# Kernel tuning notes

Measured on AMD Instinct MI355X. Metric: run time of the kernel, lower is better.

The kernel has to match this reference:

```python
import jax, jax.numpy as jnp
import numpy as np

NUM_HEADS = 16

def _rope(t, cos, sin):
    # t: [B,H,T,hd]; cos/sin: [T,half]
    half = t.shape[-1] // 2
    t1, t2 = t[..., :half], t[..., half:]
    return jnp.concatenate((t1 * cos - t2 * sin, t1 * sin + t2 * cos), axis=-1)

def setup_inputs() -> dict:
    key = jax.random.key(0)
    ks = jax.random.split(key, 5)
    B, T, D = 2, 2048, 2048
    s = 0.02
    return {
        'x': jax.random.normal(ks[0], (B, T, D), jnp.float32),
        'w_qkv': jax.random.normal(ks[1], (3 * D, D), jnp.float32) * s,
        'b_qkv': jax.random.normal(ks[2], (3 * D,), jnp.float32) * s,
        'w_out': jax.random.normal(ks[3], (D, D), jnp.float32) * s,
        'b_out': jax.random.normal(ks[4], (D,), jnp.float32) * s,
    }

def reference(x, w_qkv, b_qkv, w_out, b_out):
    B, T, D = x.shape
    H = NUM_HEADS
    hd = D // H
    half = hd // 2
    # fused QKV projection (torch Linear: x @ W^T + b)
    qkv = (x @ w_qkv.T + b_qkv).reshape(B, T, H, 3, hd)
    q, k, v = qkv[..., 0, :], qkv[..., 1, :], qkv[..., 2, :]
    q, k, v = (jnp.transpose(t, (0, 2, 1, 3)) for t in (q, k, v))  # [B,H,T,hd]
    # RoPE frequencies (buffer computed as in __init__)
    theta = 1.0 / (10000.0 ** (jnp.arange(half, dtype=jnp.float32) / half))
    freq = jnp.arange(T, dtype=jnp.float32)[:, None] * theta[None, :]  # [T,half]
    cos, sin = jnp.cos(freq), jnp.sin(freq)
    q = _rope(q, cos, sin)
    k = _rope(k, cos, sin)
    # causal attention; NOTE: source scales by embed_dim**-0.5
    scale = D ** (-0.5)
    scores = jnp.einsum('bhqd,bhkd->bhqk', q, k) * scale
    mask = jnp.triu(jnp.full((T, T), -1e9, dtype=scores.dtype), k=1)
    weights = jax.nn.softmax(scores + mask, axis=-1)
    attn = jnp.einsum('bhqk,bhkd->bhqd', weights, v)
    attn = jnp.transpose(attn, (0, 2, 1, 3)).reshape(B, T, D)
    return attn @ w_out.T + b_out
```

## Files before the change

kernel.cpp:

```cpp
#include <hip/hip_runtime.h>
#include <math.h>

#define NHEAD 16
#define TSEQ  2048
#define BATCH 2
#define DM    2048
#define QROW  6144

typedef __attribute__((ext_vector_type(8))) short bf16x8;
typedef __attribute__((ext_vector_type(4))) float f32x4;

__device__ __forceinline__ short f2bf(float f) {
    unsigned u = __builtin_bit_cast(unsigned, f);
    u += 0x7fff + ((u >> 16) & 1);
    return (short)(u >> 16);
}
__device__ __forceinline__ float bf2f(short s) {
    unsigned u = ((unsigned)(unsigned short)s) << 16;
    return __builtin_bit_cast(float, u);
}
__device__ __forceinline__ void gload_lds16(const void* g, void* l) {
    __builtin_amdgcn_global_load_lds(
        (const __attribute__((address_space(1))) unsigned int*)g,
        (__attribute__((address_space(3))) unsigned int*)l, 16, 0, 0);
}

__global__ __launch_bounds__(256)
void cast_f32_bf16(const float* __restrict__ in, short* __restrict__ out, int n)
{
    int i = (blockIdx.x * 256 + threadIdx.x) * 8;
    if (i >= n) return;
    float4 a = *(const float4*)(in + i);
    float4 b = *(const float4*)(in + i + 4);
    bf16x8 o;
    o[0]=f2bf(a.x); o[1]=f2bf(a.y); o[2]=f2bf(a.z); o[3]=f2bf(a.w);
    o[4]=f2bf(b.x); o[5]=f2bf(b.y); o[6]=f2bf(b.z); o[7]=f2bf(b.w);
    *(bf16x8*)(out + i) = o;
}

template<bool BF16_OUT>
__global__ __launch_bounds__(256)
void gemm_bf16_nt(const short* __restrict__ A, const short* __restrict__ W,
                  const float* __restrict__ bias, void* __restrict__ Cout,
                  int N, int K)
{
    __shared__ short As[128 * 64];
    __shared__ short Bs[128 * 64];
    const int tid = threadIdx.x;
    const int lane = tid & 63, w = tid >> 6;
    const int lane15 = lane & 15, quad = lane >> 4;
    const int wr = w >> 1, wc = w & 1;
    const int row0 = blockIdx.y * 128, col0 = blockIdx.x * 128;

    f32x4 acc[4][4];
    #pragma unroll
    for (int mi = 0; mi < 4; ++mi)
        #pragma unroll
        for (int ni = 0; ni < 4; ++ni)
            acc[mi][ni] = (f32x4){0.f, 0.f, 0.f, 0.f};

    for (int kt = 0; kt < K; kt += 64) {
        __syncthreads();
        #pragma unroll
        for (int i = 0; i < 4; ++i) {
            int ci = i * 256 + tid;
            int row = ci >> 3, lc = ci & 7;
            int gc = lc ^ (row & 7);
            gload_lds16(A + (size_t)(row0 + row) * K + kt + gc * 8, As + ci * 8);
            gload_lds16(W + (size_t)(col0 + row) * K + kt + gc * 8, Bs + ci * 8);
        }
        __syncthreads();
        #pragma unroll
        for (int kc = 0; kc < 2; ++kc) {
            bf16x8 af[4], bfr[4];
            #pragma unroll
            for (int mi = 0; mi < 4; ++mi) {
                int r = wr * 64 + mi * 16 + lane15;
                af[mi] = *(const bf16x8*)(As + r * 64 + ((kc * 4 + quad) ^ (r & 7)) * 8);
            }
            #pragma unroll
            for (int ni = 0; ni < 4; ++ni) {
                int r = wc * 64 + ni * 16 + lane15;
                bfr[ni] = *(const bf16x8*)(Bs + r * 64 + ((kc * 4 + quad) ^ (r & 7)) * 8);
            }
            #pragma unroll
            for (int mi = 0; mi < 4; ++mi)
                #pragma unroll
                for (int ni = 0; ni < 4; ++ni)
                    acc[mi][ni] = __builtin_amdgcn_mfma_f32_16x16x32_bf16(
                        af[mi], bfr[ni], acc[mi][ni], 0, 0, 0);
        }
    }

    #pragma unroll
    for (int mi = 0; mi < 4; ++mi) {
        #pragma unroll
        for (int ni = 0; ni < 4; ++ni) {
            int col = col0 + wc * 64 + ni * 16 + lane15;
            float bv = bias[col];
            #pragma unroll
            for (int r = 0; r < 4; ++r) {
                int row = row0 + wr * 64 + mi * 16 + quad * 4 + r;
                float v = acc[mi][ni][r] + bv;
                if (BF16_OUT) ((short*)Cout)[(size_t)row * N + col] = f2bf(v);
                else          ((float*)Cout)[(size_t)row * N + col] = v;
            }
        }
    }
}

__global__ __launch_bounds__(256)
void rope_frag(const short* __restrict__ qkvb, short* __restrict__ qfrag,
               short* __restrict__ kfrag, short* __restrict__ vfrag)
{
    __shared__ short Vsm[64 * 132];
    const int tid = threadIdx.x;
    const int lane = tid & 63, w = tid >> 6;
    const int lane15 = lane & 15, quad = lane >> 4;
    const int t0 = blockIdx.x * 64, h = blockIdx.y, b = blockIdx.z;
    const int bh = b * NHEAD + h;

    #pragma unroll
    for (int rep = 0; rep < 4; ++rep) {
        int ln = rep * 256 + tid;
        int vr = ln >> 4, c8 = (ln & 15) << 3;
        *(bf16x8*)&Vsm[vr * 132 + c8] =
            *(const bf16x8*)(qkvb + (size_t)(b * TSEQ + t0 + vr) * QROW + h * 384 + 256 + c8);
    }

    const int row = t0 + w * 16 + lane15;
    const short* rp = qkvb + (size_t)(b * TSEQ + row) * QROW + h * 384;
    bf16x8 q[4], k[4];
    #pragma unroll
    for (int kc = 0; kc < 4; ++kc) {
        q[kc] = *(const bf16x8*)(rp + kc * 32 + quad * 8);
        k[kc] = *(const bf16x8*)(rp + 128 + kc * 32 + quad * 8);
    }
    const float sc = 0.022097086912079608f;
    #pragma unroll
    for (int kc = 0; kc < 2; ++kc)
        #pragma unroll
        for (int j = 0; j < 8; ++j) {
            int d = kc * 32 + quad * 8 + j;
            float theta = exp2f(-(float)d * (13.287712379549449f / 64.0f));
            float sn, cs;
            sincosf((float)row * theta, &sn, &cs);
            float q1 = bf2f(q[kc][j]), q2 = bf2f(q[kc + 2][j]);
            float k1 = bf2f(k[kc][j]), k2 = bf2f(k[kc + 2][j]);
            q[kc][j]     = f2bf((q1 * cs - q2 * sn) * sc);
            q[kc + 2][j] = f2bf((q1 * sn + q2 * cs) * sc);
            k[kc][j]     = f2bf(k1 * cs - k2 * sn);
            k[kc + 2][j] = f2bf(k1 * sn + k2 * cs);
        }
    {
        size_t fb = (size_t)bh * 262144 + (size_t)(t0 / 16 + w) * 2048 + lane * 8;
        #pragma unroll
        for (int kc = 0; kc < 4; ++kc) {
            *(bf16x8*)(qfrag + fb + kc * 512) = q[kc];
            *(bf16x8*)(kfrag + fb + kc * 512) = k[kc];
        }
    }
    __syncthreads();
    #pragma unroll
    for (int dd = 0; dd < 2; ++dd) {
        int dt = w * 2 + dd;
        int d = dt * 16 + lane15;
        #pragma unroll
        for (int kc2 = 0; kc2 < 2; ++kc2) {
            bf16x8 vv;
            #pragma unroll
            for (int j = 0; j < 8; ++j)
                vv[j] = Vsm[(kc2 * 32 + quad * 8 + j) * 132 + d];
            *(bf16x8*)(vfrag + (size_t)bh * 262144 + (size_t)(t0 >> 6) * 8192
                        + dt * 1024 + kc2 * 512 + lane * 8) = vv;
        }
    }
}

__global__ __launch_bounds__(256, 2)
void attn2(const short* __restrict__ qfrag, const short* __restrict__ kfrag,
           const short* __restrict__ vfrag, short* __restrict__ attnb)
{
    __shared__ char smem[51200];
    short* Ks = (short*)smem;
    short* Vs = (short*)(smem + 16384);
    const int tid = threadIdx.x;
    const int lane = tid & 63, w = tid >> 6;
    const int lane15 = lane & 15, quad = lane >> 4;
    const int g = (blockIdx.x + blockIdx.y) & 15;
    const int qb = blockIdx.z ? (15 - g) : g;
    const int h = blockIdx.y, b = blockIdx.z;
    const int bh = b * NHEAD + h;
    const int q0 = qb * 128;
    short* Pscr = (short*)(smem + 32768 + w * 4608);

    bf16x8 qf[2][4];
    {
        const short* qp = qfrag + (size_t)bh * 262144
                        + (size_t)(qb * 8 + w * 2) * 2048 + lane * 8;
        #pragma unroll
        for (int nq = 0; nq < 2; ++nq)
            #pragma unroll
            for (int kc = 0; kc < 4; ++kc)
                qf[nq][kc] = *(const bf16x8*)(qp + nq * 2048 + kc * 512);
    }

    f32x4 acc[8][2];
    #pragma unroll
    for (int dt = 0; dt < 8; ++dt)
        #pragma unroll
        for (int nq = 0; nq < 2; ++nq)
            acc[dt][nq] = (f32x4){0.f, 0.f, 0.f, 0.f};
    float m_s[2] = {-3e38f, -3e38f}, l_s[2] = {0.f, 0.f};

    const short* kf_src = kfrag + (size_t)bh * 262144;
    const short* vf_src = vfrag + (size_t)bh * 262144;
    const int kb_max = (q0 + 127) >> 6;
    const int diag0 = (q0 + w * 32) >> 6;

    for (int kb = 0; kb <= kb_max; ++kb) {
        __syncthreads();
        #pragma unroll
        for (int i = 0; i < 4; ++i) {
            int ci = i * 256 + tid;
            gload_lds16(kf_src + (size_t)kb * 8192 + ci * 8, Ks + ci * 8);
            gload_lds16(vf_src + (size_t)kb * 8192 + ci * 8, Vs + ci * 8);
        }
        __syncthreads();

        f32x4 st[2][4];
        #pragma unroll
        for (int nq = 0; nq < 2; ++nq)
            #pragma unroll
            for (int mi = 0; mi < 4; ++mi)
                st[nq][mi] = (f32x4){0.f, 0.f, 0.f, 0.f};
        #pragma unroll
        for (int mi = 0; mi < 4; ++mi) {
            bf16x8 kf4[4];
            #pragma unroll
            for (int kc = 0; kc < 4; ++kc)
                kf4[kc] = *(const bf16x8*)(Ks + ((mi * 4 + kc) * 64 + lane) * 8);
            #pragma unroll
            for (int kc = 0; kc < 4; ++kc)
                #pragma unroll
                for (int nq = 0; nq < 2; ++nq)
                    st[nq][mi] = __builtin_amdgcn_mfma_f32_16x16x32_bf16(
                        kf4[kc], qf[nq][kc], st[nq][mi], 0, 0, 0);
        }

        if (kb >= diag0) {
            #pragma unroll
            for (int nq = 0; nq < 2; ++nq) {
                int qg = q0 + w * 32 + nq * 16 + lane15;
                #pragma unroll
                for (int mi = 0; mi < 4; ++mi)
                    #pragma unroll
                    for (int r = 0; r < 4; ++r)
                        if (kb * 64 + mi * 16 + quad * 4 + r > qg)
                            st[nq][mi][r] = -3e38f;
            }
        }

        #pragma unroll
        for (int nq = 0; nq < 2; ++nq) {
            float mt = st[nq][0][0];
            #pragma unroll
            for (int mi = 0; mi < 4; ++mi)
                #pragma unroll
                for (int r = 0; r < 4; ++r)
                    mt = fmaxf(mt, st[nq][mi][r]);
            mt = fmaxf(mt, __shfl_xor(mt, 16));
            mt = fmaxf(mt, __shfl_xor(mt, 32));
            float mn = fmaxf(m_s[nq], mt);
            float alpha = __expf(m_s[nq] - mn);
            m_s[nq] = mn;
            float sum = 0.f;
            #pragma unroll
            for (int mi = 0; mi < 4; ++mi)
                #pragma unroll
                for (int r = 0; r < 4; ++r) {
                    float p = __expf(st[nq][mi][r] - mn);
                    st[nq][mi][r] = p;
                    sum += p;
                }
            sum += __shfl_xor(sum, 16);
            sum += __shfl_xor(sum, 32);
            l_s[nq] = l_s[nq] * alpha + sum;
            #pragma unroll
            for (int dt = 0; dt < 8; ++dt) {
                acc[dt][nq][0] *= alpha; acc[dt][nq][1] *= alpha;
                acc[dt][nq][2] *= alpha; acc[dt][nq][3] *= alpha;
            }
            short* pr = Pscr + (nq * 16 + lane15) * 72 + quad * 4;
            #pragma unroll
            for (int mi = 0; mi < 4; ++mi) {
                unsigned lo = (unsigned)(unsigned short)f2bf(st[nq][mi][0])
                            | ((unsigned)(unsigned short)f2bf(st[nq][mi][1]) << 16);
                unsigned hi = (unsigned)(unsigned short)f2bf(st[nq][mi][2])
                            | ((unsigned)(unsigned short)f2bf(st[nq][mi][3]) << 16);
                *(unsigned*)(pr + mi * 16)     = lo;
                *(unsigned*)(pr + mi * 16 + 2) = hi;
            }
        }
        __asm__ volatile("s_waitcnt lgkmcnt(0)" ::: "memory");

        bf16x8 pb[2][2];
        #pragma unroll
        for (int nq = 0; nq < 2; ++nq)
            #pragma unroll
            for (int kc2 = 0; kc2 < 2; ++kc2)
                pb[nq][kc2] = *(const bf16x8*)
                    (Pscr + (nq * 16 + lane15) * 72 + kc2 * 32 + quad * 8);

        #pragma unroll
        for (int dt = 0; dt < 8; ++dt)
            #pragma unroll
            for (int kc2 = 0; kc2 < 2; ++kc2) {
                bf16x8 vf = *(const bf16x8*)(Vs + ((dt * 2 + kc2) * 64 + lane) * 8);
                #pragma unroll
                for (int nq = 0; nq < 2; ++nq)
                    acc[dt][nq] = __builtin_amdgcn_mfma_f32_16x16x32_bf16(
                        vf, pb[nq][kc2], acc[dt][nq], 0, 0, 0);
            }
    }

    __syncthreads();
    short* Eb = (short*)smem;
    #pragma unroll
    for (int nq = 0; nq < 2; ++nq) {
        float inv = 1.f / l_s[nq];
        int qrow = w * 32 + nq * 16 + lane15;
        #pragma unroll
        for (int dt = 0; dt < 8; ++dt) {
            unsigned lo = (unsigned)(unsigned short)f2bf(acc[dt][nq][0] * inv)
                        | ((unsigned)(unsigned short)f2bf(acc[dt][nq][1] * inv) << 16);
            unsigned hi = (unsigned)(unsigned short)f2bf(acc[dt][nq][2] * inv)
                        | ((unsigned)(unsigned short)f2bf(acc[dt][nq][3] * inv) << 16);
            *(unsigned*)(Eb + qrow * 136 + dt * 16 + quad * 4)     = lo;
            *(unsigned*)(Eb + qrow * 136 + dt * 16 + quad * 4 + 2) = hi;
        }
    }
    __syncthreads();
    {
        int r = tid >> 1, half = tid & 1;
        short* orow = attnb + (size_t)(b * TSEQ + q0 + r) * DM + h * 128 + half * 64;
        #pragma unroll
        for (int i = 0; i < 8; ++i)
            *(bf16x8*)(orow + i * 8) =
                *(const bf16x8*)(Eb + r * 136 + half * 64 + i * 8);
    }
}

extern "C" void kernel_launch(void* const* d_in, const int* in_sizes, int n_in,
                              void* d_out, int out_size, void* d_ws, size_t ws_size,
                              hipStream_t stream)
{
    const float* x     = (const float*)d_in[0];
    const float* w_qkv = (const float*)d_in[1];
    const float* b_qkv = (const float*)d_in[2];
    const float* w_out = (const float*)d_in[3];
    const float* b_out = (const float*)d_in[4];
    float* out = (float*)d_out;

    char* ws = (char*)d_ws;
    short* woutb = (short*)(ws);
    short* qkvb  = (short*)(ws + 8388608);
    short* qfrag = (short*)(ws + 58720256);
    short* kfrag = (short*)(ws + 75497472);
    short* vfrag = (short*)(ws + 92274688);
    short* xb    = (short*)(ws + 58720256);
    short* wqkvb = (short*)(ws + 75497472);
    short* attnb = qkvb;

    cast_f32_bf16<<<4096, 256, 0, stream>>>(x, xb, 8388608);
    cast_f32_bf16<<<6144, 256, 0, stream>>>(w_qkv, wqkvb, 12582912);
    cast_f32_bf16<<<2048, 256, 0, stream>>>(w_out, woutb, 4194304);

    {
        dim3 g2(6144 / 128, 4096 / 128);
        gemm_bf16_nt<true><<<g2, 256, 0, stream>>>(xb, wqkvb, b_qkv, qkvb, 6144, 2048);
    }
    {
        dim3 g2(TSEQ / 64, NHEAD, BATCH);
        rope_frag<<<g2, 256, 0, stream>>>(qkvb, qfrag, kfrag, vfrag);
    }
    {
        dim3 g2(16, NHEAD, BATCH);
        attn2<<<g2, 256, 0, stream>>>(qfrag, kfrag, vfrag, attnb);
    }
    {
        dim3 g2(2048 / 128, 4096 / 128);
        gemm_bf16_nt<false><<<g2, 256, 0, stream>>>(attnb, woutb, b_out, out, 2048, 2048);
    }
}
```

Baseline: 393.6 us.

## Fuse RoPE into QKV GEMM epilogue, merge casts, double-buffer attention K/V

The three cast kernels become one launch. RoPE and the fragment re-layout move into the QKV GEMM epilogue through shared memory, which removes the bf16 qkv intermediate and the separate rope kernel. The attention kernel now double-buffers K/V tiles with asynchronous global-to-LDS loads, and it skips blocks that lie above the causal diagonal for each wave. It also switches to fast __sincosf with manual range reduction, and it drops the occupancy hint of 2 blocks per SM, so the larger LDS footprint may reduce occupancy.

```diff
diff --git a/kernel.cpp b/kernel.cpp
--- a/kernel.cpp
+++ b/kernel.cpp
@@ -5,7 +5,6 @@
 #define TSEQ  2048
 #define BATCH 2
 #define DM    2048
-#define QROW  6144
 
 typedef __attribute__((ext_vector_type(8))) short bf16x8;
 typedef __attribute__((ext_vector_type(4))) float f32x4;
@@ -26,23 +25,152 @@
 }
 
 __global__ __launch_bounds__(256)
-void cast_f32_bf16(const float* __restrict__ in, short* __restrict__ out, int n)
+void cast_all(const float* __restrict__ x, short* __restrict__ xb,
+              const float* __restrict__ wq, short* __restrict__ wqb,
+              const float* __restrict__ wo, short* __restrict__ wob)
 {
-    int i = (blockIdx.x * 256 + threadIdx.x) * 8;
-    if (i >= n) return;
-    float4 a = *(const float4*)(in + i);
-    float4 b = *(const float4*)(in + i + 4);
+    int bid = blockIdx.x;
+    const float* src; short* dst; int lb;
+    if (bid < 4096)       { src = x;  dst = xb;  lb = bid; }
+    else if (bid < 10240) { src = wq; dst = wqb; lb = bid - 4096; }
+    else                  { src = wo; dst = wob; lb = bid - 10240; }
+    int i = (lb * 256 + threadIdx.x) * 8;
+    float4 a = *(const float4*)(src + i);
+    float4 b = *(const float4*)(src + i + 4);
     bf16x8 o;
     o[0]=f2bf(a.x); o[1]=f2bf(a.y); o[2]=f2bf(a.z); o[3]=f2bf(a.w);
     o[4]=f2bf(b.x); o[5]=f2bf(b.y); o[6]=f2bf(b.z); o[7]=f2bf(b.w);
-    *(bf16x8*)(out + i) = o;
-}
-
-template<bool BF16_OUT>
+    *(bf16x8*)(dst + i) = o;
+}
+
 __global__ __launch_bounds__(256)
-void gemm_bf16_nt(const short* __restrict__ A, const short* __restrict__ W,
-                  const float* __restrict__ bias, void* __restrict__ Cout,
-                  int N, int K)
+void gemm_qkv_rope(const short* __restrict__ A, const short* __restrict__ W,
+                   const float* __restrict__ bias, short* __restrict__ qfrag,
+                   short* __restrict__ kfrag, short* __restrict__ vfrag)
+{
+    const int K = 2048;
+    __shared__ short sm[17408];
+    short* As = sm;
+    short* Bs = sm + 8192;
+    const int tid = threadIdx.x;
+    const int lane = tid & 63, w = tid >> 6;
+    const int lane15 = lane & 15, quad = lane >> 4;
+    const int wr = w >> 1, wc = w & 1;
+    const int row0 = blockIdx.y * 128, col0 = blockIdx.x * 128;
+
+    f32x4 acc[4][4];
+    #pragma unroll
+    for (int mi = 0; mi < 4; ++mi)
+        #pragma unroll
+        for (int ni = 0; ni < 4; ++ni)
+            acc[mi][ni] = (f32x4){0.f, 0.f, 0.f, 0.f};
+
+    for (int kt = 0; kt < K; kt += 64) {
+        __syncthreads();
+        #pragma unroll
+        for (int i = 0; i < 4; ++i) {
+            int ci = i * 256 + tid;
+            int row = ci >> 3, lc = ci & 7;
+            int gc = lc ^ (row & 7);
+            gload_lds16(A + (size_t)(row0 + row) * K + kt + gc * 8, As + ci * 8);
+            gload_lds16(W + (size_t)(col0 + row) * K + kt + gc * 8, Bs + ci * 8);
+        }
+        __syncthreads();
+        #pragma unroll
+        for (int kc = 0; kc < 2; ++kc) {
+            bf16x8 af[4], bfr[4];
+            #pragma unroll
+            for (int mi = 0; mi < 4; ++mi) {
+                int r = wr * 64 + mi * 16 + lane15;
+                af[mi] = *(const bf16x8*)(As + r * 64 + ((kc * 4 + quad) ^ (r & 7)) * 8);
+            }
+            #pragma unroll
+            for (int ni = 0; ni < 4; ++ni) {
+                int r = wc * 64 + ni * 16 + lane15;
+                bfr[ni] = *(const bf16x8*)(Bs + r * 64 + ((kc * 4 + quad) ^ (r & 7)) * 8);
+            }
+            #pragma unroll
+            for (int mi = 0; mi < 4; ++mi)
+                #pragma unroll
+                for (int ni = 0; ni < 4; ++ni)
+                    acc[mi][ni] = __builtin_amdgcn_mfma_f32_16x16x32_bf16(
+                        af[mi], bfr[ni], acc[mi][ni], 0, 0, 0);
+        }
+    }
+
+    const int head = col0 / 384;
+    const int type = (col0 % 384) >> 7;
+    const int b    = row0 >> 11;
+    const int t0g  = row0 & 2047;
+    const int bh   = b * NHEAD + head;
+
+    __syncthreads();
+    #pragma unroll
+    for (int ni = 0; ni < 4; ++ni) {
+        int d = wc * 64 + ni * 16 + lane15;
+        float bv = bias[col0 + d];
+        #pragma unroll
+        for (int mi = 0; mi < 4; ++mi) {
+            int rowb = wr * 64 + mi * 16 + quad * 4;
+            #pragma unroll
+            for (int r = 0; r < 4; ++r)
+                sm[(rowb + r) * 136 + d] = f2bf(acc[mi][ni][r] + bv);
+        }
+    }
+    __syncthreads();
+
+    if (type < 2) {
+        const float sc = (type == 0) ? 0.022097086912079608f : 1.0f;
+        short* dst = (type == 0 ? qfrag : kfrag) + (size_t)bh * 262144;
+        #pragma unroll
+        for (int it = 0; it < 4; ++it) {
+            int c = it * 256 + tid;
+            int l15 = c & 15, q_ = (c >> 4) & 3, kc = (c >> 6) & 1, rowhi = c >> 7;
+            int lrow = rowhi * 16 + l15;
+            int t = t0g + lrow;
+            bf16x8 a8 = *(const bf16x8*)(sm + lrow * 136 + kc * 32 + q_ * 8);
+            bf16x8 b8 = *(const bf16x8*)(sm + lrow * 136 + kc * 32 + q_ * 8 + 64);
+            bf16x8 oa, ob;
+            #pragma unroll
+            for (int j = 0; j < 8; ++j) {
+                int d = kc * 32 + q_ * 8 + j;
+                float trev = exp2f(-(float)d * (13.287712379549449f / 64.0f))
+                             * 0.15915494309189535f;
+                float ang = (float)t * trev;
+                float fr = ang - floorf(ang);
+                float sn, cs;
+                __sincosf(fr * 6.283185307179586f, &sn, &cs);
+                float va = bf2f(a8[j]), vb = bf2f(b8[j]);
+                oa[j] = f2bf((va * cs - vb * sn) * sc);
+                ob[j] = f2bf((va * sn + vb * cs) * sc);
+            }
+            size_t base = (size_t)((t0g >> 4) + rowhi) * 2048 + (q_ * 16 + l15) * 8;
+            *(bf16x8*)(dst + base + kc * 512)        = oa;
+            *(bf16x8*)(dst + base + kc * 512 + 1024) = ob;
+        }
+    } else {
+        short* dst = vfrag + (size_t)bh * 262144;
+        #pragma unroll
+        for (int it = 0; it < 8; ++it) {
+            int c = it * 256 + tid;
+            int lane_ = c & 63, rest = c >> 6;
+            int q_ = lane_ >> 4, l15 = lane_ & 15;
+            int dt = rest & 7, kc2 = (rest >> 3) & 1, kbt = rest >> 4;
+            int d = dt * 16 + l15;
+            bf16x8 v;
+            #pragma unroll
+            for (int j = 0; j < 8; ++j)
+                v[j] = sm[(kbt * 64 + kc2 * 32 + q_ * 8 + j) * 136 + d];
+            *(bf16x8*)(dst + (size_t)((t0g >> 6) + kbt) * 8192
+                        + dt * 1024 + kc2 * 512 + lane_ * 8) = v;
+        }
+    }
+}
+
+__global__ __launch_bounds__(256)
+void gemm_out(const short* __restrict__ A, const short* __restrict__ W,
+              const float* __restrict__ bias, float* __restrict__ Cout,
+              int N, int K)
 {
     __shared__ short As[128 * 64];
     __shared__ short Bs[128 * 64];
@@ -93,7 +221,7 @@
     }
 
     #pragma unroll
-    for (int mi = 0; mi < 4; ++mi) {
+    for (int mi = 0; mi < 4; ++mi)
         #pragma unroll
         for (int ni = 0; ni < 4; ++ni) {
             int col = col0 + wc * 64 + ni * 16 + lane15;
@@ -101,89 +229,17 @@
             #pragma unroll
             for (int r = 0; r < 4; ++r) {
                 int row = row0 + wr * 64 + mi * 16 + quad * 4 + r;
-                float v = acc[mi][ni][r] + bv;
-                if (BF16_OUT) ((short*)Cout)[(size_t)row * N + col] = f2bf(v);
-                else          ((float*)Cout)[(size_t)row * N + col] = v;
-            }
-        }
-    }
+                Cout[(size_t)row * N + col] = acc[mi][ni][r] + bv;
+            }
+        }
 }
 
 __global__ __launch_bounds__(256)
-void rope_frag(const short* __restrict__ qkvb, short* __restrict__ qfrag,
-               short* __restrict__ kfrag, short* __restrict__ vfrag)
-{
-    __shared__ short Vsm[64 * 132];
-    const int tid = threadIdx.x;
-    const int lane = tid & 63, w = tid >> 6;
-    const int lane15 = lane & 15, quad = lane >> 4;
-    const int t0 = blockIdx.x * 64, h = blockIdx.y, b = blockIdx.z;
-    const int bh = b * NHEAD + h;
-
-    #pragma unroll
-    for (int rep = 0; rep < 4; ++rep) {
-        int ln = rep * 256 + tid;
-        int vr = ln >> 4, c8 = (ln & 15) << 3;
-        *(bf16x8*)&Vsm[vr * 132 + c8] =
-            *(const bf16x8*)(qkvb + (size_t)(b * TSEQ + t0 + vr) * QROW + h * 384 + 256 + c8);
-    }
-
-    const int row = t0 + w * 16 + lane15;
-    const short* rp = qkvb + (size_t)(b * TSEQ + row) * QROW + h * 384;
-    bf16x8 q[4], k[4];
-    #pragma unroll
-    for (int kc = 0; kc < 4; ++kc) {
-        q[kc] = *(const bf16x8*)(rp + kc * 32 + quad * 8);
-        k[kc] = *(const bf16x8*)(rp + 128 + kc * 32 + quad * 8);
-    }
-    const float sc = 0.022097086912079608f;
-    #pragma unroll
-    for (int kc = 0; kc < 2; ++kc)
-        #pragma unroll
-        for (int j = 0; j < 8; ++j) {
-            int d = kc * 32 + quad * 8 + j;
-            float theta = exp2f(-(float)d * (13.287712379549449f / 64.0f));
-            float sn, cs;
-            sincosf((float)row * theta, &sn, &cs);
-            float q1 = bf2f(q[kc][j]), q2 = bf2f(q[kc + 2][j]);
-            float k1 = bf2f(k[kc][j]), k2 = bf2f(k[kc + 2][j]);
-            q[kc][j]     = f2bf((q1 * cs - q2 * sn) * sc);
-            q[kc + 2][j] = f2bf((q1 * sn + q2 * cs) * sc);
-            k[kc][j]     = f2bf(k1 * cs - k2 * sn);
-            k[kc + 2][j] = f2bf(k1 * sn + k2 * cs);
-        }
-    {
-        size_t fb = (size_t)bh * 262144 + (size_t)(t0 / 16 + w) * 2048 + lane * 8;
-        #pragma unroll
-        for (int kc = 0; kc < 4; ++kc) {
-            *(bf16x8*)(qfrag + fb + kc * 512) = q[kc];
-            *(bf16x8*)(kfrag + fb + kc * 512) = k[kc];
-        }
-    }
-    __syncthreads();
-    #pragma unroll
-    for (int dd = 0; dd < 2; ++dd) {
-        int dt = w * 2 + dd;
-        int d = dt * 16 + lane15;
-        #pragma unroll
-        for (int kc2 = 0; kc2 < 2; ++kc2) {
-            bf16x8 vv;
-            #pragma unroll
-            for (int j = 0; j < 8; ++j)
-                vv[j] = Vsm[(kc2 * 32 + quad * 8 + j) * 132 + d];
-            *(bf16x8*)(vfrag + (size_t)bh * 262144 + (size_t)(t0 >> 6) * 8192
-                        + dt * 1024 + kc2 * 512 + lane * 8) = vv;
-        }
-    }
-}
-
-__global__ __launch_bounds__(256, 2)
-void attn2(const short* __restrict__ qfrag, const short* __restrict__ kfrag,
+void attn3(const short* __restrict__ qfrag, const short* __restrict__ kfrag,
            const short* __restrict__ vfrag, short* __restrict__ attnb)
 {
-    __shared__ char smem[51200];
-    short* Ks = (short*)smem;
-    short* Vs = (short*)(smem + 16384);
+    __shared__ short KV[2][16384];
+    __shared__ short Pb[4][1152];
     const int tid = threadIdx.x;
     const int lane = tid & 63, w = tid >> 6;
     const int lane15 = lane & 15, quad = lane >> 4;
@@ -192,7 +248,7 @@
     const int h = blockIdx.y, b = blockIdx.z;
     const int bh = b * NHEAD + h;
     const int q0 = qb * 128;
-    short* Pscr = (short*)(smem + 32768 + w * 4608);
+    short* Pw = Pb[w];
 
     bf16x8 qf[2][4];
     {
@@ -215,18 +271,33 @@
 
     const short* kf_src = kfrag + (size_t)bh * 262144;
     const short* vf_src = vfrag + (size_t)bh * 262144;
-    const int kb_max = (q0 + 127) >> 6;
+    const int kb_max = 2 * qb + 1;
+    const int qtop = q0 + w * 32 + 31;
     const int diag0 = (q0 + w * 32) >> 6;
+
+    #pragma unroll
+    for (int i = 0; i < 4; ++i) {
+        int ci = i * 256 + tid;
+        gload_lds16(kf_src + ci * 8, KV[0] + ci * 8);
+        gload_lds16(vf_src + ci * 8, KV[0] + 8192 + ci * 8);
+    }
 
     for (int kb = 0; kb <= kb_max; ++kb) {
         __syncthreads();
-        #pragma unroll
-        for (int i = 0; i < 4; ++i) {
-            int ci = i * 256 + tid;
-            gload_lds16(kf_src + (size_t)kb * 8192 + ci * 8, Ks + ci * 8);
-            gload_lds16(vf_src + (size_t)kb * 8192 + ci * 8, Vs + ci * 8);
-        }
-        __syncthreads();
+        if (kb < kb_max) {
+            const short* ks = kf_src + (size_t)(kb + 1) * 8192;
+            const short* vs = vf_src + (size_t)(kb + 1) * 8192;
+            short* kd = KV[(kb + 1) & 1];
+            #pragma unroll
+            for (int i = 0; i < 4; ++i) {
+                int ci = i * 256 + tid;
+                gload_lds16(ks + ci * 8, kd + ci * 8);
+                gload_lds16(vs + ci * 8, kd + 8192 + ci * 8);
+            }
+        }
+        if (kb * 64 > qtop) continue;
+        const short* Ks = KV[kb & 1];
+        const short* Vs = Ks + 8192;
 
         f32x4 st[2][4];
         #pragma unroll
@@ -261,6 +332,7 @@
             }
         }
 
+        bf16x8 pb[2][2];
         #pragma unroll
         for (int nq = 0; nq < 2; ++nq) {
             float mt = st[nq][0][0];
@@ -291,7 +363,7 @@
                 acc[dt][nq][0] *= alpha; acc[dt][nq][1] *= alpha;
                 acc[dt][nq][2] *= alpha; acc[dt][nq][3] *= alpha;
             }
-            short* pr = Pscr + (nq * 16 + lane15) * 72 + quad * 4;
+            short* pr = Pw + lane15 * 72 + quad * 4;
             #pragma unroll
             for (int mi = 0; mi < 4; ++mi) {
                 unsigned lo = (unsigned)(unsigned short)f2bf(st[nq][mi][0])
@@ -301,16 +373,12 @@
                 *(unsigned*)(pr + mi * 16)     = lo;
                 *(unsigned*)(pr + mi * 16 + 2) = hi;
             }
-        }
-        __asm__ volatile("s_waitcnt lgkmcnt(0)" ::: "memory");
-
-        bf16x8 pb[2][2];
-        #pragma unroll
-        for (int nq = 0; nq < 2; ++nq)
+            __asm__ volatile("s_waitcnt lgkmcnt(0)" ::: "memory");
             #pragma unroll
             for (int kc2 = 0; kc2 < 2; ++kc2)
-                pb[nq][kc2] = *(const bf16x8*)
-                    (Pscr + (nq * 16 + lane15) * 72 + kc2 * 32 + quad * 8);
+                pb[nq][kc2] = *(const bf16x8*)(Pw + lane15 * 72 + kc2 * 32 + quad * 8);
+            __asm__ volatile("s_waitcnt lgkmcnt(0)" ::: "memory");
+        }
 
         #pragma unroll
         for (int dt = 0; dt < 8; ++dt)
@@ -325,7 +393,7 @@
     }
 
     __syncthreads();
-    short* Eb = (short*)smem;
+    short* Eb = KV[0];
     #pragma unroll
     for (int nq = 0; nq < 2; ++nq) {
         float inv = 1.f / l_s[nq];
@@ -363,33 +431,26 @@
     float* out = (float*)d_out;
 
     char* ws = (char*)d_ws;
-    short* woutb = (short*)(ws);
-    short* qkvb  = (short*)(ws + 8388608);
-    short* qfrag = (short*)(ws + 58720256);
-    short* kfrag = (short*)(ws + 75497472);
-    short* vfrag = (short*)(ws + 92274688);
-    short* xb    = (short*)(ws + 58720256);
-    short* wqkvb = (short*)(ws + 75497472);
-    short* attnb = qkvb;
-
-    cast_f32_bf16<<<4096, 256, 0, stream>>>(x, xb, 8388608);
-    cast_f32_bf16<<<6144, 256, 0, stream>>>(w_qkv, wqkvb, 12582912);
-    cast_f32_bf16<<<2048, 256, 0, stream>>>(w_out, woutb, 4194304);
+    short* xb    = (short*)(ws);
+    short* wqkvb = (short*)(ws + 16777216);
+    short* woutb = (short*)(ws + 41943040);
+    short* qfrag = (short*)(ws + 50331648);
+    short* kfrag = (short*)(ws + 67108864);
+    short* vfrag = (short*)(ws + 83886080);
+    short* attnb = xb;
+
+    cast_all<<<12288, 256, 0, stream>>>(x, xb, w_qkv, wqkvb, w_out, woutb);
 
     {
-        dim3 g2(6144 / 128, 4096 / 128);
-        gemm_bf16_nt<true><<<g2, 256, 0, stream>>>(xb, wqkvb, b_qkv, qkvb, 6144, 2048);
-    }
-    {
-        dim3 g2(TSEQ / 64, NHEAD, BATCH);
-        rope_frag<<<g2, 256, 0, stream>>>(qkvb, qfrag, kfrag, vfrag);
+        dim3 g2(48, 32);
+        gemm_qkv_rope<<<g2, 256, 0, stream>>>(xb, wqkvb, b_qkv, qfrag, kfrag, vfrag);
     }
     {
         dim3 g2(16, NHEAD, BATCH);
-        attn2<<<g2, 256, 0, stream>>>(qfrag, kfrag, vfrag, attnb);
+        attn3<<<g2, 256, 0, stream>>>(qfrag, kfrag, vfrag, attnb);
     }
     {
-        dim3 g2(2048 / 128, 4096 / 128);
-        gemm_bf16_nt<false><<<g2, 256, 0, stream>>>(attnb, woutb, b_out, out, 2048, 2048);
-    }
-}
+        dim3 g2(16, 32);
+        gemm_out<<<g2, 256, 0, stream>>>(attnb, woutb, b_out, out, 2048, 2048);
+    }
+}
```

Measured after the change: 381.0 us. 3.2% less time.
